# Kernel optimization log

Hardware: AMD Instinct MI355X
Metric: run time of the kernel (lower is better)

The kernel has to match this reference:

```python
import jax, jax.numpy as jnp
import numpy as np

B, S, V, D = 8, 1024, 8192, 256
MAX_POS = 1024


def _positional_encoding(position, d_model):
    pos = np.arange(position)[:, None].astype(np.float32)
    i = np.arange(d_model)[None, :].astype(np.float32)
    angle_rads = pos / np.power(10000.0, 2.0 * np.floor(i / 2.0) / np.float32(d_model))
    angle_rads[:, 0::2] = np.sin(angle_rads[:, 0::2])
    angle_rads[:, 1::2] = np.cos(angle_rads[:, 1::2])
    return jnp.asarray(angle_rads[None, ...], dtype=jnp.float32)  # [1, position, d_model]


def setup_inputs() -> dict:
    key = jax.random.key(0)
    k1, k2 = jax.random.split(key)
    x = jax.random.randint(k1, (B, S, V), 0, 2, dtype=jnp.int32)  # multi-hot mask
    emb_table = jax.random.normal(k2, (V, D), dtype=jnp.float32) * 0.02
    pos_enc = _positional_encoding(MAX_POS, D)
    return {"x": x, "emb_table": emb_table, "pos_enc": pos_enc}


def reference(x, emb_table, pos_enc):
    # Multi-hot embedding-bag: sum_v x[b,s,v] * emb_table[v,:]  (dense O(V) reduction,
    # faithful to get_emb's full-vocab embed * mask + reduce_sum)
    seq_len = x.shape[1]
    d_model = emb_table.shape[1]
    xf = x.astype(jnp.float32)
    emb = jnp.einsum('bsv,vd->bsd', xf, emb_table)
    emb = emb * jnp.sqrt(jnp.float32(d_model))
    # positional encoding gated by whether the position has any active token
    any_tok = (jnp.sum(x, axis=-1) > 0).astype(jnp.float32)[..., None]  # [B,S,1]
    out = emb + pos_enc[:, :seq_len, :] * any_tok
    # dropout is identity in eval mode; num_layers = 0 -> no encoder layers
    return out
```

## Files before the change

### kernel.cpp

```cpp
#include <hip/hip_runtime.h>
#include <stdint.h>


#define K_TOT 8192
#define D_DIM 256
#define KSPLIT 4
#define KCHUNK (K_TOT / KSPLIT)
#define BK 128
#define TROWS 32
#define NTILES (KCHUNK / BK)
#define PART_STRIDE (8192u * 256u)

typedef short  short8  __attribute__((ext_vector_type(8)));
typedef float  floatx4 __attribute__((ext_vector_type(4)));
typedef int    intx4   __attribute__((ext_vector_type(4)));

union S8U { intx4 i; short8 s; };

#define WS_PART_OFF (4u * 1024u * 1024u)
#define WS_RS_OFF   (36u * 1024u * 1024u)

__device__ __forceinline__ unsigned int bf16_rne(float f) {
    unsigned int u = __float_as_uint(f);
    u += 0x7fffu + ((u >> 16) & 1u);
    return u >> 16;
}

__device__ __forceinline__ void load_lds16_nt(const int* g, int* l) {
    __builtin_amdgcn_global_load_lds((const __attribute__((address_space(1))) unsigned int*)g,
                                     (__attribute__((address_space(3))) unsigned int*)l,
                                     16, 0, 2);
}

__global__ __launch_bounds__(256) void prep_kernel(const float* __restrict__ emb,
                                                   unsigned short* __restrict__ wsBf) {
    int gid = blockIdx.x * 256 + threadIdx.x;
    int l  = gid & 63;
    int kb = (gid >> 6) & 255;
    int c  = gid >> 14;
    int d  = c * 16 + (l & 15);
    int v0 = kb * 32 + (l >> 4) * 8;
    const float* src = emb + (size_t)v0 * D_DIM + d;
    intx4 q;
#pragma unroll
    for (int p = 0; p < 4; ++p) {
        unsigned int u0 = bf16_rne(src[(size_t)(2 * p) * D_DIM] * 16.0f);
        unsigned int u1 = bf16_rne(src[(size_t)(2 * p + 1) * D_DIM] * 16.0f);
        q[p] = (int)(u0 | (u1 << 16));
    }
    *(intx4*)(wsBf + (size_t)gid * 8) = q;
}

__global__ __launch_bounds__(256) void gemm_kernel(const int* __restrict__ x,
                                                   const unsigned short* __restrict__ wsBf,
                                                   float* __restrict__ part,
                                                   int* __restrict__ rsp) {
    __shared__ int Al[2][4096];

    const int m0    = blockIdx.x * TROWS;
    const int kidx  = blockIdx.y;
    const int kbeg  = kidx * KCHUNK;
    const int phase = (blockIdx.x * 7 + blockIdx.y * 9) & (NTILES - 1);
    const int t     = threadIdx.x;
    const int wave  = t >> 6, lane = t & 63;
    const int quad  = lane >> 4, rl = lane & 15;
    const int sx    = rl & 7;

    const int srow0 = wave * 8 + (lane >> 5);
    const int slt   = lane & 31;
    const int* gsrc[4];
#pragma unroll
    for (int p = 0; p < 4; ++p) {
        int rw = srow0 + 2 * p;
        gsrc[p] = x + (size_t)(m0 + rw) * K_TOT + kbeg + ((slt ^ (rw & 7)) * 4);
    }
    const int dofs = (wave * 256 + lane) * 4;

    floatx4 acc[2][4];
#pragma unroll
    for (int i = 0; i < 2; ++i)
#pragma unroll
        for (int j = 0; j < 4; ++j) acc[i][j] = (floatx4){0.f, 0.f, 0.f, 0.f};
    int rp[2] = {0, 0};

    const int kbase = kidx * (KCHUNK / 32);

#pragma unroll
    for (int p = 0; p < 4; ++p)
        load_lds16_nt(gsrc[p] + phase * BK, &Al[0][dofs + p * 256]);

    for (int tl = 0; tl < NTILES; ++tl) {
        const int pcur = (tl + phase) & (NTILES - 1);
        __syncthreads();
        if (tl + 1 < NTILES) {
            const int pnx = (tl + 1 + phase) & (NTILES - 1);
            int* dst = &Al[(tl + 1) & 1][dofs];
#pragma unroll
            for (int p = 0; p < 4; ++p)
                load_lds16_nt(gsrc[p] + pnx * BK, dst + p * 256);
        }
        const int* buf = &Al[tl & 1][0];

#pragma unroll
        for (int s = 0; s < 4; ++s) {
            const int kb = kbase + pcur * 4 + s;

            short8 bf[4];
#pragma unroll
            for (int j = 0; j < 4; ++j)
                bf[j] = ((const S8U*)(wsBf + ((size_t)((wave * 4 + j) * 256 + kb) * 64 + lane) * 8))->s;

            short8 af[2];
#pragma unroll
            for (int i = 0; i < 2; ++i) {
                int g0 = s * 8 + quad * 2;
                int rowb = (i * 16 + rl) * 128;
                intx4 v0 = *(const intx4*)(buf + rowb + ((g0 ^ sx) * 4));
                intx4 v1 = *(const intx4*)(buf + rowb + (((g0 + 1) ^ sx) * 4));
                int p0 = v0[0] | (v0[1] << 16);
                int p1 = v0[2] | (v0[3] << 16);
                int p2 = v1[0] | (v1[1] << 16);
                int p3 = v1[2] | (v1[3] << 16);
                if (wave == 0) rp[i] += p0 + p1 + p2 + p3;
                S8U u;
                u.i[0] = p0 * 0x3F80;
                u.i[1] = p1 * 0x3F80;
                u.i[2] = p2 * 0x3F80;
                u.i[3] = p3 * 0x3F80;
                af[i] = u.s;
            }

#pragma unroll
            for (int i = 0; i < 2; ++i)
#pragma unroll
                for (int j = 0; j < 4; ++j)
                    acc[i][j] = __builtin_amdgcn_mfma_f32_16x16x32_bf16(af[i], bf[j], acc[i][j], 0, 0, 0);
        }
    }

    if (wave == 0) {
#pragma unroll
        for (int i = 0; i < 2; ++i) {
            int cnt = (rp[i] & 0xFFFF) + ((unsigned)rp[i] >> 16);
            cnt += __shfl_xor(cnt, 16);
            cnt += __shfl_xor(cnt, 32);
            if (quad == 0) rsp[(size_t)kidx * 8192 + m0 + i * 16 + rl] = cnt;
        }
    }

    float* pk = part + (size_t)kidx * PART_STRIDE;
#pragma unroll
    for (int i = 0; i < 2; ++i) {
#pragma unroll
        for (int j = 0; j < 4; ++j) {
            int col = wave * 64 + j * 16 + rl;
#pragma unroll
            for (int r = 0; r < 4; ++r) {
                int row = m0 + i * 16 + quad * 4 + r;
                __builtin_nontemporal_store(acc[i][j][r], &pk[(size_t)row * D_DIM + col]);
            }
        }
    }
}

__global__ __launch_bounds__(256) void reduce_kernel(const float* __restrict__ part,
                                                     const int* __restrict__ rsp,
                                                     const float* __restrict__ pos,
                                                     float* __restrict__ out) {
    int gid = blockIdx.x * 256 + threadIdx.x;
    size_t base = (size_t)gid * 4;
    int row = gid >> 6;
    floatx4 a = *(const floatx4*)(part + base);
    int rsum = rsp[row];
#pragma unroll
    for (int k = 1; k < KSPLIT; ++k) {
        a += *(const floatx4*)(part + (size_t)k * PART_STRIDE + base);
        rsum += rsp[(size_t)k * 8192 + row];
    }
    if (rsum > 0) {
        int s = row & 1023;
        int col = (gid & 63) * 4;
        a += *(const floatx4*)(pos + (size_t)s * D_DIM + col);
    }
    *(floatx4*)(out + base) = a;
}

extern "C" void kernel_launch(void* const* d_in, const int* in_sizes, int n_in,
                              void* d_out, int out_size, void* d_ws, size_t ws_size,
                              hipStream_t stream) {
    const int*   x   = (const int*)d_in[0];
    const float* emb = (const float*)d_in[1];
    const float* pos = (const float*)d_in[2];
    float*       out = (float*)d_out;

    unsigned short* wsBf = (unsigned short*)d_ws;
    float*          part = (float*)((char*)d_ws + WS_PART_OFF);
    int*            rsp  = (int*)((char*)d_ws + WS_RS_OFF);

    prep_kernel<<<dim3(1024), dim3(256), 0, stream>>>(emb, wsBf);
    gemm_kernel<<<dim3(256, KSPLIT), dim3(256), 0, stream>>>(x, wsBf, part, rsp);
    reduce_kernel<<<dim3(2048), dim3(256), 0, stream>>>(part, rsp, pos, out);
}
```

Baseline: 389.0 us.

## Enlarge GEMM row tile, double K-split, and store split-K partials as bf16

The GEMM block now covers 64 rows instead of 32, with a 64-wide K tile. Each block therefore reuses every loaded bf16 embedding fragment across four MFMA row groups, which halves the B-operand traffic per output row. The K dimension is split eight ways instead of four to keep the grid at 1024 blocks, and occupancy is hinted via launch bounds. To keep partial-sum traffic from doubling, partials are rounded to bf16 before storing and widened back to fp32 in the reduce kernel. This adds rounding error to every partial and fills the workspace partial region exactly.

```diff
diff --git a/kernel.cpp b/kernel.cpp
--- a/kernel.cpp
+++ b/kernel.cpp
@@ -4,16 +4,17 @@
 
 #define K_TOT 8192
 #define D_DIM 256
-#define KSPLIT 4
+#define KSPLIT 8
 #define KCHUNK (K_TOT / KSPLIT)
-#define BK 128
-#define TROWS 32
+#define BK 64
+#define TROWS 64
 #define NTILES (KCHUNK / BK)
 #define PART_STRIDE (8192u * 256u)
 
 typedef short  short8  __attribute__((ext_vector_type(8)));
 typedef float  floatx4 __attribute__((ext_vector_type(4)));
 typedef int    intx4   __attribute__((ext_vector_type(4)));
+typedef unsigned short ushort4v __attribute__((ext_vector_type(4)));
 
 union S8U { intx4 i; short8 s; };
 
@@ -51,10 +52,10 @@
     *(intx4*)(wsBf + (size_t)gid * 8) = q;
 }
 
-__global__ __launch_bounds__(256) void gemm_kernel(const int* __restrict__ x,
-                                                   const unsigned short* __restrict__ wsBf,
-                                                   float* __restrict__ part,
-                                                   int* __restrict__ rsp) {
+__global__ __launch_bounds__(256, 4) void gemm_kernel(const int* __restrict__ x,
+                                                      const unsigned short* __restrict__ wsBf,
+                                                      unsigned short* __restrict__ part,
+                                                      int* __restrict__ rsp) {
     __shared__ int Al[2][4096];
 
     const int m0    = blockIdx.x * TROWS;
@@ -66,22 +67,22 @@
     const int quad  = lane >> 4, rl = lane & 15;
     const int sx    = rl & 7;
 
-    const int srow0 = wave * 8 + (lane >> 5);
-    const int slt   = lane & 31;
+    const int srow0 = wave * 16 + (lane >> 4);
+    const int slt   = lane & 15;
     const int* gsrc[4];
 #pragma unroll
     for (int p = 0; p < 4; ++p) {
-        int rw = srow0 + 2 * p;
+        int rw = srow0 + p * 4;
         gsrc[p] = x + (size_t)(m0 + rw) * K_TOT + kbeg + ((slt ^ (rw & 7)) * 4);
     }
-    const int dofs = (wave * 256 + lane) * 4;
-
-    floatx4 acc[2][4];
-#pragma unroll
-    for (int i = 0; i < 2; ++i)
+    const int dofs = wave * 1024 + lane * 4;
+
+    floatx4 acc[4][4];
+#pragma unroll
+    for (int i = 0; i < 4; ++i)
 #pragma unroll
         for (int j = 0; j < 4; ++j) acc[i][j] = (floatx4){0.f, 0.f, 0.f, 0.f};
-    int rp[2] = {0, 0};
+    int rp[4] = {0, 0, 0, 0};
 
     const int kbase = kidx * (KCHUNK / 32);
 
@@ -102,19 +103,20 @@
         const int* buf = &Al[tl & 1][0];
 
 #pragma unroll
-        for (int s = 0; s < 4; ++s) {
-            const int kb = kbase + pcur * 4 + s;
+        for (int s = 0; s < 2; ++s) {
+            const int kb = kbase + pcur * 2 + s;
 
             short8 bf[4];
 #pragma unroll
             for (int j = 0; j < 4; ++j)
                 bf[j] = ((const S8U*)(wsBf + ((size_t)((wave * 4 + j) * 256 + kb) * 64 + lane) * 8))->s;
 
-            short8 af[2];
-#pragma unroll
-            for (int i = 0; i < 2; ++i) {
-                int g0 = s * 8 + quad * 2;
-                int rowb = (i * 16 + rl) * 128;
+            short8 af[4];
+#pragma unroll
+            for (int i = 0; i < 4; ++i) {
+                int row  = i * 16 + rl;
+                int rowb = row * 64;
+                int g0   = s * 8 + quad * 2;
                 intx4 v0 = *(const intx4*)(buf + rowb + ((g0 ^ sx) * 4));
                 intx4 v1 = *(const intx4*)(buf + rowb + (((g0 + 1) ^ sx) * 4));
                 int p0 = v0[0] | (v0[1] << 16);
@@ -131,7 +133,7 @@
             }
 
 #pragma unroll
-            for (int i = 0; i < 2; ++i)
+            for (int i = 0; i < 4; ++i)
 #pragma unroll
                 for (int j = 0; j < 4; ++j)
                     acc[i][j] = __builtin_amdgcn_mfma_f32_16x16x32_bf16(af[i], bf[j], acc[i][j], 0, 0, 0);
@@ -140,7 +142,7 @@
 
     if (wave == 0) {
 #pragma unroll
-        for (int i = 0; i < 2; ++i) {
+        for (int i = 0; i < 4; ++i) {
             int cnt = (rp[i] & 0xFFFF) + ((unsigned)rp[i] >> 16);
             cnt += __shfl_xor(cnt, 16);
             cnt += __shfl_xor(cnt, 32);
@@ -148,33 +150,37 @@
         }
     }
 
-    float* pk = part + (size_t)kidx * PART_STRIDE;
-#pragma unroll
-    for (int i = 0; i < 2; ++i) {
+    unsigned short* pk = part + (size_t)kidx * PART_STRIDE;
+#pragma unroll
+    for (int i = 0; i < 4; ++i) {
 #pragma unroll
         for (int j = 0; j < 4; ++j) {
             int col = wave * 64 + j * 16 + rl;
 #pragma unroll
             for (int r = 0; r < 4; ++r) {
                 int row = m0 + i * 16 + quad * 4 + r;
-                __builtin_nontemporal_store(acc[i][j][r], &pk[(size_t)row * D_DIM + col]);
+                __builtin_nontemporal_store((unsigned short)bf16_rne(acc[i][j][r]),
+                                            &pk[(size_t)row * D_DIM + col]);
             }
         }
     }
 }
 
-__global__ __launch_bounds__(256) void reduce_kernel(const float* __restrict__ part,
+__global__ __launch_bounds__(256) void reduce_kernel(const unsigned short* __restrict__ part,
                                                      const int* __restrict__ rsp,
                                                      const float* __restrict__ pos,
                                                      float* __restrict__ out) {
     int gid = blockIdx.x * 256 + threadIdx.x;
     size_t base = (size_t)gid * 4;
     int row = gid >> 6;
-    floatx4 a = *(const floatx4*)(part + base);
-    int rsum = rsp[row];
-#pragma unroll
-    for (int k = 1; k < KSPLIT; ++k) {
-        a += *(const floatx4*)(part + (size_t)k * PART_STRIDE + base);
+    floatx4 a = {0.f, 0.f, 0.f, 0.f};
+    int rsum = 0;
+#pragma unroll
+    for (int k = 0; k < KSPLIT; ++k) {
+        ushort4v u = *(const ushort4v*)(part + (size_t)k * PART_STRIDE + base);
+#pragma unroll
+        for (int e = 0; e < 4; ++e)
+            a[e] += __uint_as_float((unsigned int)u[e] << 16);
         rsum += rsp[(size_t)k * 8192 + row];
     }
     if (rsum > 0) {
@@ -194,10 +200,10 @@
     float*       out = (float*)d_out;
 
     unsigned short* wsBf = (unsigned short*)d_ws;
-    float*          part = (float*)((char*)d_ws + WS_PART_OFF);
+    unsigned short* part = (unsigned short*)((char*)d_ws + WS_PART_OFF);
     int*            rsp  = (int*)((char*)d_ws + WS_RS_OFF);
 
     prep_kernel<<<dim3(1024), dim3(256), 0, stream>>>(emb, wsBf);
-    gemm_kernel<<<dim3(256, KSPLIT), dim3(256), 0, stream>>>(x, wsBf, part, rsp);
+    gemm_kernel<<<dim3(128, KSPLIT), dim3(256), 0, stream>>>(x, wsBf, part, rsp);
     reduce_kernel<<<dim3(2048), dim3(256), 0, stream>>>(part, rsp, pos, out);
 }
```

New measurement: 387.5 us. About the same (-0.4%).
